# Kernel optimization log

Hardware: AMD Instinct MI355X
Metric: run time of the kernel (lower is better)

## Reference

```python
import jax, jax.numpy as jnp
import numpy as np

N_NODES = 50000
N_HEDGES = 50000
NNZ = 800000
F_IN, HID, OUT = 256, 256, 128


def setup_inputs() -> dict:
    key = jax.random.key(0)
    ks = jax.random.split(key, 8)
    x = jax.random.normal(ks[0], (N_NODES, F_IN), dtype=jnp.float32)
    vi = jax.random.randint(ks[1], (NNZ,), 0, N_NODES)
    hi = jax.random.randint(ks[2], (NNZ,), 0, N_HEDGES)
    edge_index = jnp.stack([vi, hi], axis=0).astype(jnp.int64)
    edge_weight = jnp.ones((NNZ,), dtype=jnp.float32)
    # glorot-ish init for the v2e linear weights; e2v bias zeros (bias_e2v=True)
    W1 = jax.random.normal(ks[3], (F_IN, HID), dtype=jnp.float32) / np.sqrt(F_IN)
    b1 = jnp.zeros((HID,), dtype=jnp.float32)
    W2 = jax.random.normal(ks[4], (HID, HID), dtype=jnp.float32) / np.sqrt(HID)
    b2 = jnp.zeros((HID,), dtype=jnp.float32)
    W3 = jax.random.normal(ks[5], (HID, OUT), dtype=jnp.float32) / np.sqrt(HID)
    b3 = jnp.zeros((OUT,), dtype=jnp.float32)
    return {"x": x, "edge_index": edge_index, "edge_weight": edge_weight,
            "W1": W1, "b1": b1, "W2": W2, "b2": b2, "W3": W3, "b3": b3}


def _conv(x, vi, hi, deg_v, deg_e, W, b):
    """HNN_general_conv: linear (weight_v2e) -> mean scatter v->e -> mean scatter e->v + bias (bias_e2v)."""
    msg = x @ W                                             # [N, C]
    xe = jax.ops.segment_sum(msg[vi], hi, num_segments=N_HEDGES) / deg_e  # [E, C]
    xv = jax.ops.segment_sum(xe[hi], vi, num_segments=N_NODES) / deg_v + b  # [N, C]
    return xv, xe


def reference(x, edge_index, edge_weight, W1, b1, W2, b2, W3, b3):
    vi = edge_index[0].astype(jnp.int32)
    hi = edge_index[1].astype(jnp.int32)
    ones = jnp.ones((NNZ,), dtype=x.dtype)
    deg_v = jnp.maximum(jax.ops.segment_sum(ones, vi, num_segments=N_NODES), 1.0)[:, None]
    deg_e = jnp.maximum(jax.ops.segment_sum(ones, hi, num_segments=N_HEDGES), 1.0)[:, None]
    # layer 1 and 2: conv -> ELU (dropout is identity in eval mode)
    h, _ = _conv(x, vi, hi, deg_v, deg_e, W1, b1)
    h = jax.nn.elu(h)
    h, _ = _conv(h, vi, hi, deg_v, deg_e, W2, b2)
    h = jax.nn.elu(h)
    # last layer: no activation
    out, _ = _conv(h, vi, hi, deg_v, deg_e, W3, b3)
    return out
```

## Files before the change

kernel.cpp:

```cpp
#include <hip/hip_runtime.h>
#include <math.h>

#define NN 50000
#define NE 50000
#define NNZ_E 800000
#define NBUCK 196
#define BCAP 8192
#define EPB 2048

typedef _Float16 half_t;
typedef half_t half8 __attribute__((ext_vector_type(8)));
typedef half_t half4v __attribute__((ext_vector_type(4)));
typedef float floatx4 __attribute__((ext_vector_type(4)));
typedef float floatx8 __attribute__((ext_vector_type(8)));


__global__ __launch_bounds__(256) void bin_kernel(const int* __restrict__ vi,
                                                  const int* __restrict__ hi,
                                                  int* __restrict__ bcur_e,
                                                  int* __restrict__ bcur_v,
                                                  unsigned int* __restrict__ tmp_e,
                                                  unsigned int* __restrict__ tmp_v) {
    __shared__ int cnt_e[NBUCK], cnt_v[NBUCK];
    __shared__ int gb_e[NBUCK], gb_v[NBUCK];
    int tid = threadIdx.x;
    for (int i = tid; i < NBUCK; i += 256) { cnt_e[i] = 0; cnt_v[i] = 0; }
    __syncthreads();
    int base = blockIdx.x * EPB;
    int nE = NNZ_E - base; if (nE > EPB) nE = EPB;
    int v[8], e[8], re[8], rv[8];
#pragma unroll
    for (int i = 0; i < 8; i++) {
        int off = i * 256 + tid;
        if (off < nE) {
            int k = base + off;
            v[i] = vi[k]; e[i] = hi[k];
            re[i] = atomicAdd(&cnt_e[e[i] >> 8], 1);
            rv[i] = atomicAdd(&cnt_v[v[i] >> 8], 1);
        }
    }
    __syncthreads();
    for (int i = tid; i < NBUCK; i += 256) {
        if (cnt_e[i] > 0) gb_e[i] = atomicAdd(&bcur_e[i], cnt_e[i]);
        if (cnt_v[i] > 0) gb_v[i] = atomicAdd(&bcur_v[i], cnt_v[i]);
    }
    __syncthreads();
#pragma unroll
    for (int i = 0; i < 8; i++) {
        int off = i * 256 + tid;
        if (off < nE) {
            int be = e[i] >> 8, bv = v[i] >> 8;
            tmp_e[(size_t)be * BCAP + gb_e[be] + re[i]] = ((unsigned)v[i] << 8) | (e[i] & 255);
            tmp_v[(size_t)bv * BCAP + gb_v[bv] + rv[i]] = ((unsigned)e[i] << 8) | (v[i] & 255);
        }
    }
}

__global__ __launch_bounds__(256) void fine_count(const int* __restrict__ bcur,
                                                  const unsigned int* __restrict__ tmp,
                                                  int* __restrict__ counts, int nseg) {
    __shared__ int h[256];
    int b = blockIdx.x, tid = threadIdx.x;
    h[tid] = 0;
    __syncthreads();
    int n = bcur[b];
    const unsigned int* t = tmp + (size_t)b * BCAP;
    for (int i = tid; i < n; i += 256) atomicAdd(&h[t[i] & 255], 1);
    __syncthreads();
    int seg = b * 256 + tid;
    if (seg < nseg) counts[seg] = h[tid];
}

__global__ __launch_bounds__(256) void fine_scatter(const int* __restrict__ bcur,
                                                    const unsigned int* __restrict__ tmp,
                                                    const int* __restrict__ offs,
                                                    int* __restrict__ payload, int nseg) {
    __shared__ int cur[256];
    int b = blockIdx.x, tid = threadIdx.x;
    int seg = b * 256 + tid;
    cur[tid] = (seg < nseg) ? offs[seg] : 0;
    __syncthreads();
    int n = bcur[b];
    const unsigned int* t = tmp + (size_t)b * BCAP;
    for (int i = tid; i < n; i += 256) {
        unsigned int r = t[i];
        int pos = atomicAdd(&cur[r & 255], 1);
        payload[pos] = r >> 8;
    }
}


__global__ __launch_bounds__(256) void scan_blk(const int* __restrict__ counts,
                                                int* __restrict__ offs,
                                                int* __restrict__ blocksum, int n) {
    __shared__ int sh[256];
    int tid = threadIdx.x;
    int i = blockIdx.x * 256 + tid;
    int v = (i < n) ? counts[i] : 0;
    sh[tid] = v;
    __syncthreads();
    for (int o = 1; o < 256; o <<= 1) {
        int add = (tid >= o) ? sh[tid - o] : 0;
        __syncthreads();
        sh[tid] += add;
        __syncthreads();
    }
    if (i < n) offs[i] = sh[tid] - v;
    if (tid == 255) blocksum[blockIdx.x] = sh[255];
}

__global__ __launch_bounds__(256) void scan_top(const int* __restrict__ blocksum,
                                                int* __restrict__ blockbase, int nb) {
    __shared__ int sh[256];
    int tid = threadIdx.x;
    int v = (tid < nb) ? blocksum[tid] : 0;
    sh[tid] = v;
    __syncthreads();
    for (int o = 1; o < 256; o <<= 1) {
        int add = (tid >= o) ? sh[tid - o] : 0;
        __syncthreads();
        sh[tid] += add;
        __syncthreads();
    }
    if (tid < nb) blockbase[tid] = sh[tid] - v;
}

__global__ void scan_fix(const int* __restrict__ counts, const int* __restrict__ blockbase,
                         int* __restrict__ offs, float* __restrict__ inv, int n) {
    int i = blockIdx.x * 256 + threadIdx.x;
    if (i < n) {
        offs[i] = offs[i] + blockbase[i >> 8];
        inv[i] = 1.0f / fmaxf((float)counts[i], 1.0f);
    }
}


__global__ void cvt_split(const float* __restrict__ X, half_t* __restrict__ Xh,
                          half_t* __restrict__ Xl, int n) {
    int i = (blockIdx.x * 256 + threadIdx.x) * 4;
    if (i < n) {
        float4 v = *(const float4*)(X + i);
        half4v h, l;
        h.x = (half_t)v.x; l.x = (half_t)(v.x - (float)h.x);
        h.y = (half_t)v.y; l.y = (half_t)(v.y - (float)h.y);
        h.z = (half_t)v.z; l.z = (half_t)(v.z - (float)h.z);
        h.w = (half_t)v.w; l.w = (half_t)(v.w - (float)h.w);
        *(half4v*)(Xh + i) = h;
        *(half4v*)(Xl + i) = l;
    }
}

__global__ void cvt_w(const float* __restrict__ W, half_t* __restrict__ Wth,
                      half_t* __restrict__ Wtl, int Kd, int Nd) {
    int idx = blockIdx.x * 256 + threadIdx.x;
    if (idx < Kd * Nd) {
        int k = idx / Nd, n = idx - k * Nd;
        float v = W[idx];
        half_t h = (half_t)v;
        Wth[(size_t)n * Kd + k] = h;
        Wtl[(size_t)n * Kd + k] = (half_t)(v - (float)h);
    }
}


#define LSTR 40

__global__ __launch_bounds__(256) void gemm_hsplit(const half_t* __restrict__ Ah,
                                                   const half_t* __restrict__ Al,
                                                   const half_t* __restrict__ Bh,
                                                   const half_t* __restrict__ Bl,
                                                   half_t* __restrict__ C,
                                                   int M, int N, int K) {
    __shared__ __attribute__((aligned(16))) half_t sAh[128 * LSTR];
    __shared__ __attribute__((aligned(16))) half_t sAl[128 * LSTR];
    __shared__ __attribute__((aligned(16))) half_t sBh[128 * LSTR];
    __shared__ __attribute__((aligned(16))) half_t sBl[128 * LSTR];

    int tid = threadIdx.x;
    int wave = tid >> 6, lane = tid & 63;
    int row0 = blockIdx.y * 128, col0 = blockIdx.x * 128;
    int qm = (wave >> 1) * 64, qn = (wave & 1) * 64;

    int sr = tid >> 1;
    int sk = (tid & 1) * 16;
    int fm = lane & 15;
    int fk = (lane >> 4) * 8;

    floatx4 acc[4][4] = {};

    for (int k0 = 0; k0 < K; k0 += 32) {
        half8 a0 = {}, a1 = {}, l0 = {}, l1 = {};
        int arow = row0 + sr;
        if (arow < M) {
            const half_t* pa = Ah + (size_t)arow * K + k0 + sk;
            const half_t* pl = Al + (size_t)arow * K + k0 + sk;
            a0 = *(const half8*)pa; a1 = *(const half8*)(pa + 8);
            l0 = *(const half8*)pl; l1 = *(const half8*)(pl + 8);
        }
        *(half8*)&sAh[sr * LSTR + sk]     = a0;
        *(half8*)&sAh[sr * LSTR + sk + 8] = a1;
        *(half8*)&sAl[sr * LSTR + sk]     = l0;
        *(half8*)&sAl[sr * LSTR + sk + 8] = l1;
        {
            const half_t* pb = Bh + (size_t)(col0 + sr) * K + k0 + sk;
            const half_t* pc = Bl + (size_t)(col0 + sr) * K + k0 + sk;
            half8 b0 = *(const half8*)pb, b1 = *(const half8*)(pb + 8);
            half8 c0 = *(const half8*)pc, c1 = *(const half8*)(pc + 8);
            *(half8*)&sBh[sr * LSTR + sk]     = b0;
            *(half8*)&sBh[sr * LSTR + sk + 8] = b1;
            *(half8*)&sBl[sr * LSTR + sk]     = c0;
            *(half8*)&sBl[sr * LSTR + sk + 8] = c1;
        }
        __syncthreads();

        half8 fa_h[4], fa_l[4], fb_h[4], fb_l[4];
#pragma unroll
        for (int i = 0; i < 4; i++) {
            fa_h[i] = *(const half8*)&sAh[(qm + i * 16 + fm) * LSTR + fk];
            fa_l[i] = *(const half8*)&sAl[(qm + i * 16 + fm) * LSTR + fk];
            fb_h[i] = *(const half8*)&sBh[(qn + i * 16 + fm) * LSTR + fk];
            fb_l[i] = *(const half8*)&sBl[(qn + i * 16 + fm) * LSTR + fk];
        }
#pragma unroll
        for (int mi = 0; mi < 4; mi++)
#pragma unroll
            for (int ni = 0; ni < 4; ni++) {
                acc[mi][ni] = __builtin_amdgcn_mfma_f32_16x16x32_f16(fa_h[mi], fb_h[ni], acc[mi][ni], 0, 0, 0);
                acc[mi][ni] = __builtin_amdgcn_mfma_f32_16x16x32_f16(fa_h[mi], fb_l[ni], acc[mi][ni], 0, 0, 0);
                acc[mi][ni] = __builtin_amdgcn_mfma_f32_16x16x32_f16(fa_l[mi], fb_h[ni], acc[mi][ni], 0, 0, 0);
            }
        __syncthreads();
    }

    int er = (lane >> 4) * 4;
    int ec = lane & 15;
#pragma unroll
    for (int mi = 0; mi < 4; mi++)
#pragma unroll
        for (int r = 0; r < 4; r++) {
            int grow = row0 + qm + mi * 16 + er + r;
            if (grow < M) {
#pragma unroll
                for (int ni = 0; ni < 4; ni++)
                    C[(size_t)grow * N + col0 + qn + ni * 16 + ec] = (half_t)acc[mi][ni][r];
            }
        }
}


template <int LPR, int MODE>
__global__ __launch_bounds__(256) void seg16(const half_t* __restrict__ src,
                                             const int* __restrict__ offs,
                                             const int* __restrict__ counts,
                                             const int* __restrict__ payload,
                                             const float* __restrict__ inv,
                                             const float* __restrict__ bias,
                                             half_t* __restrict__ dst_h,
                                             half_t* __restrict__ dst_l,
                                             float* __restrict__ dst_f,
                                             int nrows) {
    const int C = LPR * 8;
    int gtid = blockIdx.x * 256 + threadIdx.x;
    int row = gtid / LPR;
    if (row >= nrows) return;
    int c0 = (gtid % LPR) * 8;
    int start = offs[row], cnt = counts[row];
    int j = start, end = start + cnt;
    floatx8 a0 = {}, a1 = {}, a2 = {}, a3 = {};
    for (; j + 4 <= end; j += 4) {
        int s0 = payload[j], s1 = payload[j + 1], s2 = payload[j + 2], s3 = payload[j + 3];
        half8 v0 = *(const half8*)(src + (size_t)s0 * C + c0);
        half8 v1 = *(const half8*)(src + (size_t)s1 * C + c0);
        half8 v2 = *(const half8*)(src + (size_t)s2 * C + c0);
        half8 v3 = *(const half8*)(src + (size_t)s3 * C + c0);
        a0 += __builtin_convertvector(v0, floatx8);
        a1 += __builtin_convertvector(v1, floatx8);
        a2 += __builtin_convertvector(v2, floatx8);
        a3 += __builtin_convertvector(v3, floatx8);
    }
    for (; j < end; j++) {
        int sr = payload[j];
        half8 v = *(const half8*)(src + (size_t)sr * C + c0);
        a0 += __builtin_convertvector(v, floatx8);
    }
    floatx8 acc = (a0 + a1) + (a2 + a3);
    acc *= inv[row];
    if (MODE >= 1) {
        float4 b0 = *(const float4*)(bias + c0);
        float4 b1 = *(const float4*)(bias + c0 + 4);
        acc[0] += b0.x; acc[1] += b0.y; acc[2] += b0.z; acc[3] += b0.w;
        acc[4] += b1.x; acc[5] += b1.y; acc[6] += b1.z; acc[7] += b1.w;
    }
    if (MODE == 1) {
#pragma unroll
        for (int k = 0; k < 8; k++) acc[k] = acc[k] > 0.f ? acc[k] : expm1f(acc[k]);
        half8 h = __builtin_convertvector(acc, half8);
        floatx8 back = __builtin_convertvector(h, floatx8);
        half8 l = __builtin_convertvector(acc - back, half8);
        *(half8*)(dst_h + (size_t)row * C + c0) = h;
        *(half8*)(dst_l + (size_t)row * C + c0) = l;
    } else if (MODE == 0) {
        *(half8*)(dst_h + (size_t)row * C + c0) = __builtin_convertvector(acc, half8);
    } else {
        float* o = dst_f + (size_t)row * C + c0;
        *(float4*)o = make_float4(acc[0], acc[1], acc[2], acc[3]);
        *(float4*)(o + 4) = make_float4(acc[4], acc[5], acc[6], acc[7]);
    }
}


extern "C" void kernel_launch(void* const* d_in, const int* in_sizes, int n_in,
                              void* d_out, int out_size, void* d_ws, size_t ws_size,
                              hipStream_t stream) {
    const float* x  = (const float*)d_in[0];
    const int*   ei = (const int*)d_in[1];
    const int* vi = ei;
    const int* hi = ei + NNZ_E;
    const float* W1 = (const float*)d_in[3];
    const float* b1 = (const float*)d_in[4];
    const float* W2 = (const float*)d_in[5];
    const float* b2 = (const float*)d_in[6];
    const float* W3 = (const float*)d_in[7];
    const float* b3 = (const float*)d_in[8];
    float* out = (float*)d_out;

    char* p = (char*)d_ws;
    auto take = [&](size_t bytes) -> void* {
        void* r = (void*)p;
        p += (bytes + 255) & ~(size_t)255;
        return r;
    };
    const int NB = (NN + 255) / 256;
    int* counts_v = (int*)take(NN * 4);
    int* counts_e = (int*)take(NE * 4);
    int* offs_v   = (int*)take(NN * 4);
    int* offs_e   = (int*)take(NE * 4);
    int* bsum_v   = (int*)take(NB * 4);
    int* bsum_e   = (int*)take(NB * 4);
    int* bbase_v  = (int*)take(NB * 4);
    int* bbase_e  = (int*)take(NB * 4);
    int* bcur_e   = (int*)take(NBUCK * 4);
    int* bcur_v   = (int*)take(NBUCK * 4);
    unsigned int* tmp_e = (unsigned int*)take((size_t)NBUCK * BCAP * 4);
    unsigned int* tmp_v = (unsigned int*)take((size_t)NBUCK * BCAP * 4);
    int* pay_v    = (int*)take((size_t)NNZ_E * 4);
    int* pay_e    = (int*)take((size_t)NNZ_E * 4);
    float* inv_v  = (float*)take(NN * 4);
    float* inv_e  = (float*)take(NE * 4);
    half_t* msgH  = (half_t*)take((size_t)NN * 256 * 2);
    half_t* xeH   = (half_t*)take((size_t)NE * 256 * 2);
    half_t* hA_h  = (half_t*)take((size_t)NN * 256 * 2);
    half_t* hA_l  = (half_t*)take((size_t)NN * 256 * 2);
    half_t* w1h   = (half_t*)take(256 * 256 * 2);
    half_t* w1l   = (half_t*)take(256 * 256 * 2);
    half_t* w2h   = (half_t*)take(256 * 256 * 2);
    half_t* w2l   = (half_t*)take(256 * 256 * 2);
    half_t* w3h   = (half_t*)take(256 * 128 * 2);
    half_t* w3l   = (half_t*)take(256 * 128 * 2);

    hipMemsetAsync(bcur_e, 0, NBUCK * 4, stream);
    hipMemsetAsync(bcur_v, 0, NBUCK * 4, stream);
    bin_kernel<<<(NNZ_E + EPB - 1) / EPB, 256, 0, stream>>>(vi, hi, bcur_e, bcur_v, tmp_e, tmp_v);
    fine_count<<<NBUCK, 256, 0, stream>>>(bcur_e, tmp_e, counts_e, NE);
    fine_count<<<NBUCK, 256, 0, stream>>>(bcur_v, tmp_v, counts_v, NN);
    scan_blk<<<NB, 256, 0, stream>>>(counts_v, offs_v, bsum_v, NN);
    scan_blk<<<NB, 256, 0, stream>>>(counts_e, offs_e, bsum_e, NE);
    scan_top<<<1, 256, 0, stream>>>(bsum_v, bbase_v, NB);
    scan_top<<<1, 256, 0, stream>>>(bsum_e, bbase_e, NB);
    scan_fix<<<NB, 256, 0, stream>>>(counts_v, bbase_v, offs_v, inv_v, NN);
    scan_fix<<<NB, 256, 0, stream>>>(counts_e, bbase_e, offs_e, inv_e, NE);
    fine_scatter<<<NBUCK, 256, 0, stream>>>(bcur_e, tmp_e, offs_e, pay_e, NE);
    fine_scatter<<<NBUCK, 256, 0, stream>>>(bcur_v, tmp_v, offs_v, pay_v, NN);

    cvt_split<<<(NN * 256 / 4 + 255) / 256, 256, 0, stream>>>(x, hA_h, hA_l, NN * 256);
    cvt_w<<<(256 * 256 + 255) / 256, 256, 0, stream>>>(W1, w1h, w1l, 256, 256);
    cvt_w<<<(256 * 256 + 255) / 256, 256, 0, stream>>>(W2, w2h, w2l, 256, 256);
    cvt_w<<<(256 * 128 + 255) / 256, 256, 0, stream>>>(W3, w3h, w3l, 256, 128);

    dim3 g256(2, (NN + 127) / 128);
    dim3 g128(1, (NN + 127) / 128);
    int gridC256 = (NN * 32 + 255) / 256;
    int gridC128 = (NN * 16 + 255) / 256;

    gemm_hsplit<<<g256, 256, 0, stream>>>(hA_h, hA_l, w1h, w1l, msgH, NN, 256, 256);
    seg16<32, 0><<<gridC256, 256, 0, stream>>>(msgH, offs_e, counts_e, pay_e, inv_e,
                                               nullptr, xeH, nullptr, nullptr, NE);
    seg16<32, 1><<<gridC256, 256, 0, stream>>>(xeH, offs_v, counts_v, pay_v, inv_v,
                                               b1, hA_h, hA_l, nullptr, NN);
    gemm_hsplit<<<g256, 256, 0, stream>>>(hA_h, hA_l, w2h, w2l, msgH, NN, 256, 256);
    seg16<32, 0><<<gridC256, 256, 0, stream>>>(msgH, offs_e, counts_e, pay_e, inv_e,
                                               nullptr, xeH, nullptr, nullptr, NE);
    seg16<32, 1><<<gridC256, 256, 0, stream>>>(xeH, offs_v, counts_v, pay_v, inv_v,
                                               b2, hA_h, hA_l, nullptr, NN);
    gemm_hsplit<<<g128, 256, 0, stream>>>(hA_h, hA_l, w3h, w3l, msgH, NN, 128, 256);
    seg16<16, 0><<<gridC128, 256, 0, stream>>>(msgH, offs_e, counts_e, pay_e, inv_e,
                                               nullptr, xeH, nullptr, nullptr, NE);
    seg16<16, 2><<<gridC128, 256, 0, stream>>>(xeH, offs_v, counts_v, pay_v, inv_v,
                                               b3, nullptr, nullptr, out, NN);
}
```

Before: 576.5 us.

## Store activations in 32-channel chunk-major layout so gathers stay in cache

All intermediate half-precision activations are stored chunk-major: 32-channel slabs of 64 bytes per row, with all rows of one slab contiguous. Each segment-sum block handles one channel chunk for 64 rows. The gathered working set per chunk (about 3.2 MB) can then stay resident in L2/MALL while the random gathers run. The GEMM input loads, the GEMM output stores and the conversion kernel are changed to match. Nontemporal loads and stores are added for payload indices and outputs. The cost is that every gather is now 16 bytes with four lanes per row, so each row's index list is reread once per chunk.

Measured after the change: 699.6 us. +21.4%, slower.

```diff
diff --git a/kernel.cpp b/kernel.cpp
--- a/kernel.cpp
+++ b/kernel.cpp
@@ -136,17 +136,19 @@
 
 
 __global__ void cvt_split(const float* __restrict__ X, half_t* __restrict__ Xh,
-                          half_t* __restrict__ Xl, int n) {
+                          half_t* __restrict__ Xl, int nrows) {
     int i = (blockIdx.x * 256 + threadIdx.x) * 4;
-    if (i < n) {
+    if (i < nrows * 256) {
         float4 v = *(const float4*)(X + i);
         half4v h, l;
         h.x = (half_t)v.x; l.x = (half_t)(v.x - (float)h.x);
         h.y = (half_t)v.y; l.y = (half_t)(v.y - (float)h.y);
         h.z = (half_t)v.z; l.z = (half_t)(v.z - (float)h.z);
         h.w = (half_t)v.w; l.w = (half_t)(v.w - (float)h.w);
-        *(half4v*)(Xh + i) = h;
-        *(half4v*)(Xl + i) = l;
+        int row = i >> 8, ch = i & 255;
+        size_t di = (size_t)(ch >> 5) * nrows * 32 + (size_t)row * 32 + (ch & 31);
+        *(half4v*)(Xh + di) = h;
+        *(half4v*)(Xl + di) = l;
     }
 }
 
@@ -191,11 +193,11 @@
     for (int k0 = 0; k0 < K; k0 += 32) {
         half8 a0 = {}, a1 = {}, l0 = {}, l1 = {};
         int arow = row0 + sr;
+        int kk = k0 + sk;
         if (arow < M) {
-            const half_t* pa = Ah + (size_t)arow * K + k0 + sk;
-            const half_t* pl = Al + (size_t)arow * K + k0 + sk;
-            a0 = *(const half8*)pa; a1 = *(const half8*)(pa + 8);
-            l0 = *(const half8*)pl; l1 = *(const half8*)(pl + 8);
+            size_t ai = (size_t)(kk >> 5) * M * 32 + (size_t)arow * 32 + (kk & 31);
+            a0 = *(const half8*)(Ah + ai); a1 = *(const half8*)(Ah + ai + 8);
+            l0 = *(const half8*)(Al + ai); l1 = *(const half8*)(Al + ai + 8);
         }
         *(half8*)&sAh[sr * LSTR + sk]     = a0;
         *(half8*)&sAh[sr * LSTR + sk + 8] = a1;
@@ -241,14 +243,17 @@
             int grow = row0 + qm + mi * 16 + er + r;
             if (grow < M) {
 #pragma unroll
-                for (int ni = 0; ni < 4; ni++)
-                    C[(size_t)grow * N + col0 + qn + ni * 16 + ec] = (half_t)acc[mi][ni][r];
+                for (int ni = 0; ni < 4; ni++) {
+                    int col = col0 + qn + ni * 16 + ec;
+                    size_t ci = (size_t)(col >> 5) * M * 32 + (size_t)grow * 32 + (col & 31);
+                    __builtin_nontemporal_store((half_t)acc[mi][ni][r], C + ci);
+                }
             }
         }
 }
 
 
-template <int LPR, int MODE>
+template <int NCHUNK, int MODE>
 __global__ __launch_bounds__(256) void seg16(const half_t* __restrict__ src,
                                              const int* __restrict__ offs,
                                              const int* __restrict__ counts,
@@ -258,36 +263,42 @@
                                              half_t* __restrict__ dst_h,
                                              half_t* __restrict__ dst_l,
                                              float* __restrict__ dst_f,
-                                             int nrows) {
-    const int C = LPR * 8;
-    int gtid = blockIdx.x * 256 + threadIdx.x;
-    int row = gtid / LPR;
+                                             int nrows, int nsrc) {
+    int chunk = blockIdx.x % NCHUNK;
+    int grp = blockIdx.x / NCHUNK;
+    int tid = threadIdx.x;
+    int row = grp * 64 + (tid >> 2);
     if (row >= nrows) return;
-    int c0 = (gtid % LPR) * 8;
+    int co = (tid & 3) * 8;
+    const half_t* sbase = src + (size_t)chunk * nsrc * 32 + co;
     int start = offs[row], cnt = counts[row];
     int j = start, end = start + cnt;
     floatx8 a0 = {}, a1 = {}, a2 = {}, a3 = {};
     for (; j + 4 <= end; j += 4) {
-        int s0 = payload[j], s1 = payload[j + 1], s2 = payload[j + 2], s3 = payload[j + 3];
-        half8 v0 = *(const half8*)(src + (size_t)s0 * C + c0);
-        half8 v1 = *(const half8*)(src + (size_t)s1 * C + c0);
-        half8 v2 = *(const half8*)(src + (size_t)s2 * C + c0);
-        half8 v3 = *(const half8*)(src + (size_t)s3 * C + c0);
+        int s0 = __builtin_nontemporal_load(payload + j);
+        int s1 = __builtin_nontemporal_load(payload + j + 1);
+        int s2 = __builtin_nontemporal_load(payload + j + 2);
+        int s3 = __builtin_nontemporal_load(payload + j + 3);
+        half8 v0 = *(const half8*)(sbase + (size_t)s0 * 32);
+        half8 v1 = *(const half8*)(sbase + (size_t)s1 * 32);
+        half8 v2 = *(const half8*)(sbase + (size_t)s2 * 32);
+        half8 v3 = *(const half8*)(sbase + (size_t)s3 * 32);
         a0 += __builtin_convertvector(v0, floatx8);
         a1 += __builtin_convertvector(v1, floatx8);
         a2 += __builtin_convertvector(v2, floatx8);
         a3 += __builtin_convertvector(v3, floatx8);
     }
     for (; j < end; j++) {
-        int sr = payload[j];
-        half8 v = *(const half8*)(src + (size_t)sr * C + c0);
+        int sr = __builtin_nontemporal_load(payload + j);
+        half8 v = *(const half8*)(sbase + (size_t)sr * 32);
         a0 += __builtin_convertvector(v, floatx8);
     }
     floatx8 acc = (a0 + a1) + (a2 + a3);
     acc *= inv[row];
+    int gch = chunk * 32 + co;
     if (MODE >= 1) {
-        float4 b0 = *(const float4*)(bias + c0);
-        float4 b1 = *(const float4*)(bias + c0 + 4);
+        float4 b0 = *(const float4*)(bias + gch);
+        float4 b1 = *(const float4*)(bias + gch + 4);
         acc[0] += b0.x; acc[1] += b0.y; acc[2] += b0.z; acc[3] += b0.w;
         acc[4] += b1.x; acc[5] += b1.y; acc[6] += b1.z; acc[7] += b1.w;
     }
@@ -297,14 +308,18 @@
         half8 h = __builtin_convertvector(acc, half8);
         floatx8 back = __builtin_convertvector(h, floatx8);
         half8 l = __builtin_convertvector(acc - back, half8);
-        *(half8*)(dst_h + (size_t)row * C + c0) = h;
-        *(half8*)(dst_l + (size_t)row * C + c0) = l;
+        size_t di = (size_t)chunk * nrows * 32 + (size_t)row * 32 + co;
+        __builtin_nontemporal_store(h, (half8*)(dst_h + di));
+        __builtin_nontemporal_store(l, (half8*)(dst_l + di));
     } else if (MODE == 0) {
-        *(half8*)(dst_h + (size_t)row * C + c0) = __builtin_convertvector(acc, half8);
+        size_t di = (size_t)chunk * nrows * 32 + (size_t)row * 32 + co;
+        __builtin_nontemporal_store(__builtin_convertvector(acc, half8), (half8*)(dst_h + di));
     } else {
-        float* o = dst_f + (size_t)row * C + c0;
-        *(float4*)o = make_float4(acc[0], acc[1], acc[2], acc[3]);
-        *(float4*)(o + 4) = make_float4(acc[4], acc[5], acc[6], acc[7]);
+        float* o = dst_f + (size_t)row * (NCHUNK * 32) + gch;
+        floatx4 lo = {acc[0], acc[1], acc[2], acc[3]};
+        floatx4 hi4 = {acc[4], acc[5], acc[6], acc[7]};
+        __builtin_nontemporal_store(lo, (floatx4*)o);
+        __builtin_nontemporal_store(hi4, (floatx4*)(o + 4));
     }
 }
 
@@ -372,29 +387,30 @@
     fine_scatter<<<NBUCK, 256, 0, stream>>>(bcur_e, tmp_e, offs_e, pay_e, NE);
     fine_scatter<<<NBUCK, 256, 0, stream>>>(bcur_v, tmp_v, offs_v, pay_v, NN);
 
-    cvt_split<<<(NN * 256 / 4 + 255) / 256, 256, 0, stream>>>(x, hA_h, hA_l, NN * 256);
+    cvt_split<<<(NN * 256 / 4 + 255) / 256, 256, 0, stream>>>(x, hA_h, hA_l, NN);
     cvt_w<<<(256 * 256 + 255) / 256, 256, 0, stream>>>(W1, w1h, w1l, 256, 256);
     cvt_w<<<(256 * 256 + 255) / 256, 256, 0, stream>>>(W2, w2h, w2l, 256, 256);
     cvt_w<<<(256 * 128 + 255) / 256, 256, 0, stream>>>(W3, w3h, w3l, 256, 128);
 
     dim3 g256(2, (NN + 127) / 128);
     dim3 g128(1, (NN + 127) / 128);
-    int gridC256 = (NN * 32 + 255) / 256;
-    int gridC128 = (NN * 16 + 255) / 256;
+    int grpN = (NN + 63) / 64;
+    int gridC256 = 8 * grpN;
+    int gridC128 = 4 * grpN;
 
     gemm_hsplit<<<g256, 256, 0, stream>>>(hA_h, hA_l, w1h, w1l, msgH, NN, 256, 256);
-    seg16<32, 0><<<gridC256, 256, 0, stream>>>(msgH, offs_e, counts_e, pay_e, inv_e,
-                                               nullptr, xeH, nullptr, nullptr, NE);
-    seg16<32, 1><<<gridC256, 256, 0, stream>>>(xeH, offs_v, counts_v, pay_v, inv_v,
-                                               b1, hA_h, hA_l, nullptr, NN);
+    seg16<8, 0><<<gridC256, 256, 0, stream>>>(msgH, offs_e, counts_e, pay_e, inv_e,
+                                              nullptr, xeH, nullptr, nullptr, NE, NN);
+    seg16<8, 1><<<gridC256, 256, 0, stream>>>(xeH, offs_v, counts_v, pay_v, inv_v,
+                                              b1, hA_h, hA_l, nullptr, NN, NE);
     gemm_hsplit<<<g256, 256, 0, stream>>>(hA_h, hA_l, w2h, w2l, msgH, NN, 256, 256);
-    seg16<32, 0><<<gridC256, 256, 0, stream>>>(msgH, offs_e, counts_e, pay_e, inv_e,
-                                               nullptr, xeH, nullptr, nullptr, NE);
-    seg16<32, 1><<<gridC256, 256, 0, stream>>>(xeH, offs_v, counts_v, pay_v, inv_v,
-                                               b2, hA_h, hA_l, nullptr, NN);
+    seg16<8, 0><<<gridC256, 256, 0, stream>>>(msgH, offs_e, counts_e, pay_e, inv_e,
+                                              nullptr, xeH, nullptr, nullptr, NE, NN);
+    seg16<8, 1><<<gridC256, 256, 0, stream>>>(xeH, offs_v, counts_v, pay_v, inv_v,
+                                              b2, hA_h, hA_l, nullptr, NN, NE);
     gemm_hsplit<<<g128, 256, 0, stream>>>(hA_h, hA_l, w3h, w3l, msgH, NN, 128, 256);
-    seg16<16, 0><<<gridC128, 256, 0, stream>>>(msgH, offs_e, counts_e, pay_e, inv_e,
-                                               nullptr, xeH, nullptr, nullptr, NE);
-    seg16<16, 2><<<gridC128, 256, 0, stream>>>(xeH, offs_v, counts_v, pay_v, inv_v,
-                                               b3, nullptr, nullptr, out, NN);
-}
+    seg16<4, 0><<<gridC128, 256, 0, stream>>>(msgH, offs_e, counts_e, pay_e, inv_e,
+                                              nullptr, xeH, nullptr, nullptr, NE, NN);
+    seg16<4, 2><<<gridC128, 256, 0, stream>>>(xeH, offs_v, counts_v, pay_v, inv_v,
+                                              b3, nullptr, nullptr, out, NN, NE);
+}
```
